# Performance work log

Hardware: AMD Instinct MI355X
Metric: run time of the kernel (lower is better)

Reference implementation:

```python
import jax, jax.numpy as jnp
import numpy as np

N, S, P = 262144, 128, 64
LOSS_WEIGHT = 1.0
EPS = np.float32(np.finfo(np.float32).eps)  # lossfun_outer default eps


def setup_inputs() -> dict:
    key = jax.random.key(0)
    k_t, k_w, k_th, k_wh = jax.random.split(key, 4)
    # fine bin edges strictly inside (0,1), sorted along last dim
    t = jnp.sort(jax.random.uniform(k_t, (N, S + 1), minval=1e-4, maxval=1.0 - 1e-4), axis=-1)
    w = jax.random.uniform(k_w, (N, S))
    # proposal bin edges: fixed endpoints 0 and 1 so all t fall inside -> in-range indices
    inner = jnp.sort(jax.random.uniform(k_th, (N, P - 1)), axis=-1)
    t_hat = jnp.concatenate([jnp.zeros((N, 1)), inner, jnp.ones((N, 1))], axis=-1)  # [N, P+1]
    w_hat = jax.random.uniform(k_wh, (N, P))
    return {"t": t, "w": w, "t_hat": t_hat, "w_hat": w_hat}


def _inner_outer(t0, t1, y1):
    # cy1: [N, P+1] prefix sums with leading zero
    cy1 = jnp.concatenate([jnp.zeros_like(y1[..., :1]), jnp.cumsum(y1, axis=-1)], axis=-1)
    # batched binary searches (row-wise sorted t1)
    idx_left = jax.vmap(lambda a, v: jnp.searchsorted(a, v, side='left'))(t1, t0)
    idx_right = jax.vmap(lambda a, v: jnp.searchsorted(a, v, side='right'))(t1, t0)
    cy1_lo = jnp.take_along_axis(cy1, idx_left, axis=-1)   # [N, S+1]
    cy1_hi = jnp.take_along_axis(cy1, idx_right, axis=-1)  # [N, S+1]
    return cy1_hi[..., 1:] - cy1_lo[..., :-1]              # [N, S]


def reference(t, w, t_hat, w_hat):
    w_outer = _inner_outer(t, t_hat, w_hat)
    loss = jnp.maximum(0.0, w - w_outer) ** 2 / (w + EPS)
    return LOSS_WEIGHT * loss  # [N, S], no reduction (matches forward)
```

## Files before the change

kernel.cpp:

```cpp
#include <hip/hip_runtime.h>

namespace {

constexpr int S = 128;
constexpr int P = 64;
constexpr float EPS = 1.1920928955078125e-07f;

__device__ inline float bperm_f(int byteaddr, float v) {
    return __int_as_float(__builtin_amdgcn_ds_bpermute(byteaddr, __float_as_int(v)));
}

template <int CTRL, int ROW_MASK>
__device__ inline float dpp_add(float v) {
    int perm = __builtin_amdgcn_update_dpp(0, __float_as_int(v), CTRL, ROW_MASK, 0xf, false);
    return v + __int_as_float(perm);
}

template <int LANE>
__device__ inline float rdlane_f(float v) {
    return __int_as_float(__builtin_amdgcn_readlane(__float_as_int(v), LANE));
}

__global__ __launch_bounds__(256) void proposal_loss_kernel(
    const float* __restrict__ t,
    const float* __restrict__ w,
    const float* __restrict__ t_hat,
    const float* __restrict__ w_hat,
    float* __restrict__ out)
{
    const int wv   = threadIdx.x >> 6;
    const int lane = threadIdx.x & 63;
    const int row  = (blockIdx.x << 2) + wv;

    const float* t_row  = t     + (size_t)row * (S + 1);
    const float* w_row  = w     + (size_t)row * S;
    const float* th_row = t_hat + (size_t)row * (P + 1);
    const float* wh_row = w_hat + (size_t)row * P;
    float*       o_row  = out   + (size_t)row * S;

    const float  th1 = th_row[lane + 1];
    const float  wh  = wh_row[lane];
    const float2 tt  = *reinterpret_cast<const float2*>(t_row + 2 * lane);
    const float2 ww  = *reinterpret_cast<const float2*>(w_row + 2 * lane);
    const float  t2  = t_row[2 * lane + 2];

    float inc = wh;
    inc = dpp_add<0x111, 0xf>(inc);
    inc = dpp_add<0x112, 0xf>(inc);
    inc = dpp_add<0x114, 0xf>(inc);
    inc = dpp_add<0x118, 0xf>(inc);
    inc = dpp_add<0x142, 0xa>(inc);
    inc = dpp_add<0x143, 0xc>(inc);

    const float e31 = rdlane_f<31>(th1);
    const float e15 = rdlane_f<15>(th1);
    const float e47 = rdlane_f<47>(th1);
    const float e7  = rdlane_f<7>(th1);
    const float e23 = rdlane_f<23>(th1);
    const float e39 = rdlane_f<39>(th1);
    const float e55 = rdlane_f<55>(th1);

    auto lbb = [&](float v) {
        int posb = (e31 < v) ? 128 : 0;
        float l2 = posb ? e47 : e15;
        posb += (l2 < v) ? 64 : 0;
        float l3a = (posb & 128) ? e39 : e7;
        float l3b = (posb & 128) ? e55 : e23;
        float l3  = (posb & 64) ? l3b : l3a;
        posb += (l3 < v) ? 32 : 0;
        float p = bperm_f(posb + 12, th1);  posb += (p < v) ? 16 : 0;
        p = bperm_f(posb + 4, th1);         posb += (p < v) ? 8 : 0;
        p = bperm_f(posb, th1);             posb += (p < v) ? 4 : 0;
        return posb;
    };

    const float t0  = tt.x;
    const float t1v = tt.y;
    const int b0 = lbb(t0);
    const int b1 = lbb(t1v);
    const int b2 = lbb(t2);

    const float q1 = th_row[(b1 >> 2) + 1];
    const float q2 = th_row[(b2 >> 2) + 1];
    const int r1b = b1 + ((q1 == t1v) ? 4 : 0);
    const int r2b = b2 + ((q2 == t2) ? 4 : 0);

    const float cy_l0 = bperm_f(b0,  inc);
    const float cy_l1 = bperm_f(b1,  inc);
    const float cy_r1 = bperm_f(r1b, inc);
    const float cy_r2 = bperm_f(r2b, inc);

    const float wo0 = cy_r1 - cy_l0;
    const float wo1 = cy_r2 - cy_l1;

    const float d0 = fmaxf(0.0f, ww.x - wo0);
    const float d1 = fmaxf(0.0f, ww.y - wo1);
    float2 res;
    res.x = d0 * d0 * __builtin_amdgcn_rcpf(ww.x + EPS);
    res.y = d1 * d1 * __builtin_amdgcn_rcpf(ww.y + EPS);
    *reinterpret_cast<float2*>(o_row + 2 * lane) = res;
}

}

extern "C" void kernel_launch(void* const* d_in, const int* in_sizes, int n_in,
                              void* d_out, int out_size, void* d_ws, size_t ws_size,
                              hipStream_t stream) {
    const float* t     = (const float*)d_in[0];
    const float* w     = (const float*)d_in[1];
    const float* t_hat = (const float*)d_in[2];
    const float* w_hat = (const float*)d_in[3];
    float* out = (float*)d_out;

    const int N = in_sizes[1] / S;
    proposal_loss_kernel<<<N / 4, 256, 0, stream>>>(t, w, t_hat, w_hat, out);
}
```

Baseline: 102.1 us.

## Process two rows per wave and reuse neighbor searches via shuffle

Each wave now handles two rows, with all global loads for both rows issued up front to raise memory-level parallelism, and the grid is halved. The third binary search per lane (for t[2*lane+2]) is dropped: the right-side index comes from the neighbor lane's left search via shfl_down, plus a ballot/popcount for the last edge. The dependent global loads of t_hat used for the equality check are replaced with ds_bpermute reads from registers. This trades more registers per thread, and possibly lower occupancy, for fewer instructions and fewer dependent memory round trips.

```diff
diff --git a/kernel.cpp b/kernel.cpp
--- a/kernel.cpp
+++ b/kernel.cpp
@@ -30,75 +30,93 @@
 {
     const int wv   = threadIdx.x >> 6;
     const int lane = threadIdx.x & 63;
-    const int row  = (blockIdx.x << 2) + wv;
+    const int row0 = (blockIdx.x << 3) + (wv << 1);
 
-    const float* t_row  = t     + (size_t)row * (S + 1);
-    const float* w_row  = w     + (size_t)row * S;
-    const float* th_row = t_hat + (size_t)row * (P + 1);
-    const float* wh_row = w_hat + (size_t)row * P;
-    float*       o_row  = out   + (size_t)row * S;
+    float  th1[2], wh[2], tS[2];
+    float2 tt[2], ww[2];
 
-    const float  th1 = th_row[lane + 1];
-    const float  wh  = wh_row[lane];
-    const float2 tt  = *reinterpret_cast<const float2*>(t_row + 2 * lane);
-    const float2 ww  = *reinterpret_cast<const float2*>(w_row + 2 * lane);
-    const float  t2  = t_row[2 * lane + 2];
+    #pragma unroll
+    for (int r = 0; r < 2; ++r) {
+        const int row = row0 + r;
+        const float* t_row  = t     + (size_t)row * (S + 1);
+        const float* w_row  = w     + (size_t)row * S;
+        const float* th_row = t_hat + (size_t)row * (P + 1);
+        const float* wh_row = w_hat + (size_t)row * P;
+        th1[r] = th_row[lane + 1];
+        wh[r]  = wh_row[lane];
+        tt[r]  = *reinterpret_cast<const float2*>(t_row + 2 * lane);
+        ww[r]  = *reinterpret_cast<const float2*>(w_row + 2 * lane);
+        tS[r]  = t_row[S];
+    }
 
-    float inc = wh;
-    inc = dpp_add<0x111, 0xf>(inc);
-    inc = dpp_add<0x112, 0xf>(inc);
-    inc = dpp_add<0x114, 0xf>(inc);
-    inc = dpp_add<0x118, 0xf>(inc);
-    inc = dpp_add<0x142, 0xa>(inc);
-    inc = dpp_add<0x143, 0xc>(inc);
+    float2 res[2];
 
-    const float e31 = rdlane_f<31>(th1);
-    const float e15 = rdlane_f<15>(th1);
-    const float e47 = rdlane_f<47>(th1);
-    const float e7  = rdlane_f<7>(th1);
-    const float e23 = rdlane_f<23>(th1);
-    const float e39 = rdlane_f<39>(th1);
-    const float e55 = rdlane_f<55>(th1);
+    #pragma unroll
+    for (int r = 0; r < 2; ++r) {
+        float inc = wh[r];
+        inc = dpp_add<0x111, 0xf>(inc);
+        inc = dpp_add<0x112, 0xf>(inc);
+        inc = dpp_add<0x114, 0xf>(inc);
+        inc = dpp_add<0x118, 0xf>(inc);
+        inc = dpp_add<0x142, 0xa>(inc);
+        inc = dpp_add<0x143, 0xc>(inc);
 
-    auto lbb = [&](float v) {
-        int posb = (e31 < v) ? 128 : 0;
-        float l2 = posb ? e47 : e15;
-        posb += (l2 < v) ? 64 : 0;
-        float l3a = (posb & 128) ? e39 : e7;
-        float l3b = (posb & 128) ? e55 : e23;
-        float l3  = (posb & 64) ? l3b : l3a;
-        posb += (l3 < v) ? 32 : 0;
-        float p = bperm_f(posb + 12, th1);  posb += (p < v) ? 16 : 0;
-        p = bperm_f(posb + 4, th1);         posb += (p < v) ? 8 : 0;
-        p = bperm_f(posb, th1);             posb += (p < v) ? 4 : 0;
-        return posb;
-    };
+        const float e31 = rdlane_f<31>(th1[r]);
+        const float e15 = rdlane_f<15>(th1[r]);
+        const float e47 = rdlane_f<47>(th1[r]);
+        const float e7  = rdlane_f<7 >(th1[r]);
+        const float e23 = rdlane_f<23>(th1[r]);
+        const float e39 = rdlane_f<39>(th1[r]);
+        const float e55 = rdlane_f<55>(th1[r]);
 
-    const float t0  = tt.x;
-    const float t1v = tt.y;
-    const int b0 = lbb(t0);
-    const int b1 = lbb(t1v);
-    const int b2 = lbb(t2);
+        auto lbb = [&](float v) {
+            int posb = (e31 < v) ? 128 : 0;
+            float l2 = posb ? e47 : e15;
+            posb += (l2 < v) ? 64 : 0;
+            float l3a = (posb & 128) ? e39 : e7;
+            float l3b = (posb & 128) ? e55 : e23;
+            float l3  = (posb & 64) ? l3b : l3a;
+            posb += (l3 < v) ? 32 : 0;
+            float p = bperm_f(posb + 12, th1[r]);  posb += (p < v) ? 16 : 0;
+            p = bperm_f(posb + 4, th1[r]);         posb += (p < v) ? 8 : 0;
+            p = bperm_f(posb, th1[r]);             posb += (p < v) ? 4 : 0;
+            return posb;
+        };
 
-    const float q1 = th_row[(b1 >> 2) + 1];
-    const float q2 = th_row[(b2 >> 2) + 1];
-    const int r1b = b1 + ((q1 == t1v) ? 4 : 0);
-    const int r2b = b2 + ((q2 == t2) ? 4 : 0);
+        const float t0  = tt[r].x;
+        const float t1v = tt[r].y;
+        const int b0 = lbb(t0);
+        const int b1 = lbb(t1v);
 
-    const float cy_l0 = bperm_f(b0,  inc);
-    const float cy_l1 = bperm_f(b1,  inc);
-    const float cy_r1 = bperm_f(r1b, inc);
-    const float cy_r2 = bperm_f(r2b, inc);
+        const float p0 = bperm_f(b0, th1[r]);
+        const float p1 = bperm_f(b1, th1[r]);
+        const int u0b = b0 + ((p0 == t0)  ? 4 : 0);
+        const int u1b = b1 + ((p1 == t1v) ? 4 : 0);
 
-    const float wo0 = cy_r1 - cy_l0;
-    const float wo1 = cy_r2 - cy_l1;
+        int r2b = __shfl_down(u0b, 1, 64);
+        const unsigned long long mS = __ballot(th1[r] <= tS[r]);
+        const int pcb = (int)__popcll(mS) << 2;
+        if (lane == 63) r2b = pcb;
 
-    const float d0 = fmaxf(0.0f, ww.x - wo0);
-    const float d1 = fmaxf(0.0f, ww.y - wo1);
-    float2 res;
-    res.x = d0 * d0 * __builtin_amdgcn_rcpf(ww.x + EPS);
-    res.y = d1 * d1 * __builtin_amdgcn_rcpf(ww.y + EPS);
-    *reinterpret_cast<float2*>(o_row + 2 * lane) = res;
+        const float cy_l0 = bperm_f(b0,  inc);
+        const float cy_l1 = bperm_f(b1,  inc);
+        const float cy_h0 = bperm_f(u1b, inc);
+        const float cy_h1 = bperm_f(r2b, inc);
+
+        const float wo0 = cy_h0 - cy_l0;
+        const float wo1 = cy_h1 - cy_l1;
+
+        const float d0 = fmaxf(0.0f, ww[r].x - wo0);
+        const float d1 = fmaxf(0.0f, ww[r].y - wo1);
+        res[r].x = d0 * d0 * __builtin_amdgcn_rcpf(ww[r].x + EPS);
+        res[r].y = d1 * d1 * __builtin_amdgcn_rcpf(ww[r].y + EPS);
+    }
+
+    #pragma unroll
+    for (int r = 0; r < 2; ++r) {
+        float* o_row = out + (size_t)(row0 + r) * S;
+        *reinterpret_cast<float2*>(o_row + 2 * lane) = res[r];
+    }
 }
 
 }
@@ -113,5 +131,5 @@
     float* out = (float*)d_out;
 
     const int N = in_sizes[1] / S;
-    proposal_loss_kernel<<<N / 4, 256, 0, stream>>>(t, w, t_hat, w_hat, out);
+    proposal_loss_kernel<<<N / 8, 256, 0, stream>>>(t, w, t_hat, w_hat, out);
 }
```

Result: faster. 98.64 us (-3.4%).
